# Optimization experiments

Measured on AMD Instinct MI355X. Metric: run time of the kernel, lower is better.

Reference implementation:

```python
import jax, jax.numpy as jnp
import numpy as np

B, S, D, H, HD = 2, 2048, 2048, 16, 128


def precompute_freqs_cis(dim, end, theta=10000.0):
    freqs = 1.0 / theta ** (np.arange(0, dim, 2, dtype=np.float32)[: dim // 2] / dim)
    t = np.arange(end, dtype=np.float32)
    freqs = np.outer(t, freqs)
    freqs = np.concatenate((freqs, freqs), axis=-1)  # [S, HD]
    return jnp.asarray(np.cos(freqs)), jnp.asarray(np.sin(freqs))


def rotate_half(x):
    x1, x2 = x[..., : x.shape[-1] // 2], x[..., x.shape[-1] // 2 :]
    return jnp.concatenate((-x2, x1), axis=-1)


def setup_inputs() -> dict:
    key = jax.random.key(0)
    ks = jax.random.split(key, 5)
    scale = 1.0 / np.sqrt(D)
    return {
        "x": jax.random.normal(ks[0], (B, S, D), jnp.float32),
        "mask": jnp.ones((1, 1, S, S), jnp.bool_),
        "Wq": jax.random.normal(ks[1], (D, H, HD), jnp.float32) * scale,
        "Wk": jax.random.normal(ks[2], (D, H, HD), jnp.float32) * scale,
        "Wv": jax.random.normal(ks[3], (D, H, HD), jnp.float32) * scale,
        "Wo": jax.random.normal(ks[4], (H, HD, D), jnp.float32) * scale,
    }


def reference(x, mask, Wq, Wk, Wv, Wo):
    seq_len = x.shape[1]
    head_dim = Wq.shape[-1]
    # QKV projections: [B,S,D] x [D,H,HD] -> [B,S,H,HD]
    q = jnp.einsum("bsd,dhk->bshk", x, Wq)
    k = jnp.einsum("bsd,dhk->bshk", x, Wk)
    v = jnp.einsum("bsd,dhk->bshk", x, Wv)
    # Rotary position embedding
    cos, sin = precompute_freqs_cis(head_dim, seq_len)
    cos = cos[None, :, None, :]  # [1,S,1,HD]
    sin = sin[None, :, None, :]
    q = q * cos + rotate_half(q) * sin
    k = k * cos + rotate_half(k) * sin
    # Scaled dot-product attention (flax dot_product_attention semantics)
    scores = jnp.einsum("bqhk,bskh->bhqs", q / jnp.sqrt(jnp.float32(head_dim)), k.swapaxes(-1, -2))
    big_neg = jnp.finfo(scores.dtype).min
    scores = jnp.where(mask, scores, big_neg)
    attn = jax.nn.softmax(scores, axis=-1)  # [B,H,S,S]
    ctx = jnp.einsum("bhqs,bshk->bqhk", attn, v)  # [B,S,H,HD]
    # Output projection over (head, head_dim)
    return jnp.einsum("bqhk,hkd->bqd", ctx, Wo)
```

## Files before the change

### kernel.cpp

```cpp
#include <hip/hip_runtime.h>
#include <math.h>

#define Bc   2
#define Sc   2048
#define Dc   2048
#define Hc   16
#define HDc  128
#define BSc  4096
#define HHDc 2048

typedef __bf16 bf16_t;
typedef __bf16 bf16x8 __attribute__((ext_vector_type(8)));
typedef __bf16 bf16x4 __attribute__((ext_vector_type(4)));
typedef float  f32x4  __attribute__((ext_vector_type(4)));

#define AS1(p) ((const __attribute__((address_space(1))) void*)(p))
#define AS3(p) ((__attribute__((address_space(3))) void*)(p))

#define MFMA16(a,b,c) __builtin_amdgcn_mfma_f32_16x16x32_bf16((a),(b),(c),0,0,0)

__global__ void convert_x(const float* __restrict__ x, bf16_t* __restrict__ xb)
{
    const size_t i = ((size_t)blockIdx.x * 256 + threadIdx.x) * 4;
    float4 v = *(const float4*)&x[i];
    bf16x4 o; o[0]=(bf16_t)v.x; o[1]=(bf16_t)v.y; o[2]=(bf16_t)v.z; o[3]=(bf16_t)v.w;
    *(bf16x4*)&xb[i] = o;
}

__global__ __launch_bounds__(256) void transpose_w(const float* __restrict__ in,
                                                   bf16_t* __restrict__ out)
{
    __shared__ float T[64][65];
    const int t = threadIdx.x;
    const int r0 = blockIdx.y * 64, c0 = blockIdx.x * 64;
    #pragma unroll
    for (int i = 0; i < 4; ++i) {
        int row = i * 16 + (t >> 4);
        int c4  = (t & 15) * 4;
        float4 v = *(const float4*)&in[(size_t)(r0 + row) * 2048 + c0 + c4];
        T[row][c4] = v.x; T[row][c4+1] = v.y; T[row][c4+2] = v.z; T[row][c4+3] = v.w;
    }
    __syncthreads();
    #pragma unroll
    for (int i = 0; i < 4; ++i) {
        int orow = i * 16 + (t >> 4);
        int c4   = (t & 15) * 4;
        bf16x4 o;
        #pragma unroll
        for (int j = 0; j < 4; ++j) o[j] = (bf16_t)T[c4 + j][orow];
        *(bf16x4*)&out[(size_t)(c0 + orow) * 2048 + r0 + c4] = o;
    }
}

__global__ __launch_bounds__(256) void prep_vtb(const bf16_t* __restrict__ V,
                                                bf16_t* __restrict__ Vt)
{
    __shared__ float T[64][65];
    const int t = threadIdx.x;
    const int s0 = blockIdx.x * 64;
    const int c0 = blockIdx.y * 64;
    const int bh = blockIdx.z;
    const int b = bh >> 4, h = bh & 15;
    #pragma unroll
    for (int i = 0; i < 4; ++i) {
        int row = i * 16 + (t >> 4);
        int c4  = (t & 15) * 4;
        bf16x4 v = *(const bf16x4*)&V[((size_t)(b * Sc + s0 + row)) * HHDc + h * HDc + c0 + c4];
        #pragma unroll
        for (int j = 0; j < 4; ++j) T[row][c4 + j] = (float)v[j];
    }
    __syncthreads();
    #pragma unroll
    for (int i = 0; i < 4; ++i) {
        int orow = i * 16 + (t >> 4);
        int c4   = (t & 15) * 4;
        bf16x4 o;
        #pragma unroll
        for (int j = 0; j < 4; ++j) o[j] = (bf16_t)T[c4 + j][orow];
        *(bf16x4*)&Vt[((size_t)bh * HDc + c0 + orow) * Sc + s0 + c4] = o;
    }
}

__global__ __launch_bounds__(256) void qkv_gemm(const bf16_t* __restrict__ A,
                                                const bf16_t* __restrict__ Bt,
                                                float* __restrict__ Qf,
                                                float* __restrict__ Kf,
                                                bf16_t* __restrict__ Vb)
{
    __shared__ bf16_t As[128 * 64];
    __shared__ bf16_t Bs[128 * 64];
    const int t = threadIdx.x;
    const int w = t >> 6, l = t & 63;
    const int wm = w >> 1, wn = w & 1;
    const int lane15 = l & 15, quad = l >> 4;
    const int swr = (lane15 & 7) * 8;
    const int m0 = blockIdx.y * 128, n0 = blockIdx.x * 128;

    f32x4 acc[4][4];
    #pragma unroll
    for (int i = 0; i < 4; ++i)
        #pragma unroll
        for (int j = 0; j < 4; ++j)
            #pragma unroll
            for (int c = 0; c < 4; ++c) acc[i][j][c] = 0.f;

    const int srow = w * 8 + (l >> 3);
    const int gk   = ((l & 7) * 8) ^ ((srow & 7) * 8);

    for (int k0 = 0; k0 < 2048; k0 += 64) {
        __syncthreads();
        #pragma unroll
        for (int p = 0; p < 4; ++p) {
            __builtin_amdgcn_global_load_lds(
                AS1(A + (size_t)(m0 + p * 32 + srow) * 2048 + k0 + gk),
                AS3(&As[(p * 32 + w * 8) * 64]), 16, 0, 0);
            __builtin_amdgcn_global_load_lds(
                AS1(Bt + (size_t)(n0 + p * 32 + srow) * 2048 + k0 + gk),
                AS3(&Bs[(p * 32 + w * 8) * 64]), 16, 0, 0);
        }
        __syncthreads();
        #pragma unroll
        for (int ks = 0; ks < 2; ++ks) {
            const int rc = ((ks * 4 + quad) * 8) ^ swr;
            bf16x8 a[4], b[4];
            #pragma unroll
            for (int mt = 0; mt < 4; ++mt)
                a[mt] = *(const bf16x8*)&As[(wm * 64 + mt * 16 + lane15) * 64 + rc];
            #pragma unroll
            for (int nt = 0; nt < 4; ++nt)
                b[nt] = *(const bf16x8*)&Bs[(wn * 64 + nt * 16 + lane15) * 64 + rc];
            #pragma unroll
            for (int mt = 0; mt < 4; ++mt)
                #pragma unroll
                for (int nt = 0; nt < 4; ++nt)
                    acc[mt][nt] = MFMA16(a[mt], b[nt], acc[mt][nt]);
        }
    }

    if (n0 < 4096) {
        float* __restrict__ dst = (n0 < 2048) ? Qf : Kf;
        const int nb = n0 & 2047;
        #pragma unroll
        for (int mt = 0; mt < 4; ++mt)
            #pragma unroll
            for (int nt = 0; nt < 4; ++nt)
                #pragma unroll
                for (int r = 0; r < 4; ++r) {
                    const int gm = m0 + wm * 64 + mt * 16 + quad * 4 + r;
                    const int gn = nb + wn * 64 + nt * 16 + lane15;
                    dst[(size_t)gm * 2048 + gn] = acc[mt][nt][r];
                }
    } else {
        const int nb = n0 - 4096;
        #pragma unroll
        for (int mt = 0; mt < 4; ++mt)
            #pragma unroll
            for (int nt = 0; nt < 4; ++nt)
                #pragma unroll
                for (int r = 0; r < 4; ++r) {
                    const int gm = m0 + wm * 64 + mt * 16 + quad * 4 + r;
                    const int gn = nb + wn * 64 + nt * 16 + lane15;
                    Vb[(size_t)gm * 2048 + gn] = (bf16_t)acc[mt][nt][r];
                }
    }
}

__global__ __launch_bounds__(256) void gemm_bt(const bf16_t* __restrict__ A,
                                               const bf16_t* __restrict__ Bt,
                                               float* __restrict__ C)
{
    __shared__ bf16_t As[128 * 64];
    __shared__ bf16_t Bs[128 * 64];
    const int t = threadIdx.x;
    const int w = t >> 6, l = t & 63;
    const int wm = w >> 1, wn = w & 1;
    const int lane15 = l & 15, quad = l >> 4;
    const int swr = (lane15 & 7) * 8;
    const int m0 = blockIdx.y * 128, n0 = blockIdx.x * 128;

    f32x4 acc[4][4];
    #pragma unroll
    for (int i = 0; i < 4; ++i)
        #pragma unroll
        for (int j = 0; j < 4; ++j)
            #pragma unroll
            for (int c = 0; c < 4; ++c) acc[i][j][c] = 0.f;

    const int srow = w * 8 + (l >> 3);
    const int gk   = ((l & 7) * 8) ^ ((srow & 7) * 8);

    for (int k0 = 0; k0 < 2048; k0 += 64) {
        __syncthreads();
        #pragma unroll
        for (int p = 0; p < 4; ++p) {
            __builtin_amdgcn_global_load_lds(
                AS1(A + (size_t)(m0 + p * 32 + srow) * 2048 + k0 + gk),
                AS3(&As[(p * 32 + w * 8) * 64]), 16, 0, 0);
            __builtin_amdgcn_global_load_lds(
                AS1(Bt + (size_t)(n0 + p * 32 + srow) * 2048 + k0 + gk),
                AS3(&Bs[(p * 32 + w * 8) * 64]), 16, 0, 0);
        }
        __syncthreads();
        #pragma unroll
        for (int ks = 0; ks < 2; ++ks) {
            const int rc = ((ks * 4 + quad) * 8) ^ swr;
            bf16x8 a[4], b[4];
            #pragma unroll
            for (int mt = 0; mt < 4; ++mt)
                a[mt] = *(const bf16x8*)&As[(wm * 64 + mt * 16 + lane15) * 64 + rc];
            #pragma unroll
            for (int nt = 0; nt < 4; ++nt)
                b[nt] = *(const bf16x8*)&Bs[(wn * 64 + nt * 16 + lane15) * 64 + rc];
            #pragma unroll
            for (int mt = 0; mt < 4; ++mt)
                #pragma unroll
                for (int nt = 0; nt < 4; ++nt)
                    acc[mt][nt] = MFMA16(a[mt], b[nt], acc[mt][nt]);
        }
    }

    #pragma unroll
    for (int mt = 0; mt < 4; ++mt)
        #pragma unroll
        for (int nt = 0; nt < 4; ++nt)
            #pragma unroll
            for (int r = 0; r < 4; ++r) {
                const int gm = m0 + wm * 64 + mt * 16 + quad * 4 + r;
                const int gn = n0 + wn * 64 + nt * 16 + lane15;
                C[(size_t)gm * 2048 + gn] = acc[mt][nt][r];
            }
}

__global__ void rope_scale_cast(const float* __restrict__ Qf,
                                const float* __restrict__ Kf,
                                bf16_t* __restrict__ Qh,
                                bf16_t* __restrict__ Kh)
{
    const int idx  = blockIdx.x * 256 + threadIdx.x;
    const int j4   = (idx & 15) * 4;
    const int h    = (idx >> 4) & (Hc - 1);
    const int sabs = idx >> 8;
    const int s    = sabs & (Sc - 1);
    const float QS = 0.08838834764831845f;

    const size_t base = (size_t)sabs * HHDc + (size_t)h * HDc + j4;
    float4 q1 = *(const float4*)&Qf[base];
    float4 q2 = *(const float4*)&Qf[base + 64];
    float4 k1 = *(const float4*)&Kf[base];
    float4 k2 = *(const float4*)&Kf[base + 64];

    bf16x4 qo1, qo2, ko1, ko2;
    #pragma unroll
    for (int c = 0; c < 4; ++c) {
        const float freq = expf(-(float)(j4 + c) * 0.14391156514261520f);
        const float ang  = (float)s * freq;
        float sn, cs;
        sincosf(ang, &sn, &cs);
        const float a = ((const float*)&q1)[c], bq = ((const float*)&q2)[c];
        const float x = ((const float*)&k1)[c], y  = ((const float*)&k2)[c];
        qo1[c] = (bf16_t)((a * cs - bq * sn) * QS);
        qo2[c] = (bf16_t)((bq * cs + a * sn) * QS);
        ko1[c] = (bf16_t)(x * cs - y * sn);
        ko2[c] = (bf16_t)(y * cs + x * sn);
    }
    *(bf16x4*)&Qh[base]      = qo1;
    *(bf16x4*)&Qh[base + 64] = qo2;
    *(bf16x4*)&Kh[base]      = ko1;
    *(bf16x4*)&Kh[base + 64] = ko2;
}

__global__ __launch_bounds__(512, 4) void attn_v6(const bf16_t* __restrict__ Q,
                                                  const bf16_t* __restrict__ K,
                                                  const bf16_t* __restrict__ Vt,
                                                  bf16_t* __restrict__ CTX)
{
    __shared__ bf16_t Ks[64 * 128];
    __shared__ bf16_t Vts[128 * 64];
    __shared__ bf16_t Ps[128 * 72];
    __shared__ float  Arow[128];
    __shared__ float  Lrow[128];

    const int t = threadIdx.x, w = t >> 6, l = t & 63;
    const int lane15 = l & 15, quad = l >> 4;
    const int swr = (lane15 & 7) * 8;
    const int q0 = blockIdx.x * 128;
    const int b = blockIdx.y >> 4, h = blockIdx.y & 15;
    const size_t qbase = ((size_t)(b * Sc + q0)) * HHDc + h * HDc;
    const size_t vtb   = (size_t)blockIdx.y * HDc * Sc;
    const size_t kb0   = ((size_t)(b * Sc)) * HHDc + h * HDc;

    bf16x8 qf[4];
    #pragma unroll
    for (int ks = 0; ks < 4; ++ks)
        qf[ks] = *(const bf16x8*)&Q[qbase
            + (size_t)(w * 16 + lane15) * HHDc + (ks * 4 + quad) * 8];

    float m_[4], l_[4];
    #pragma unroll
    for (int r = 0; r < 4; ++r) { m_[r] = -INFINITY; l_[r] = 0.f; }

    f32x4 O[8];
    #pragma unroll
    for (int i = 0; i < 8; ++i)
        #pragma unroll
        for (int c = 0; c < 4; ++c) O[i][c] = 0.f;

    const int krow0 = w * 4 + (l >> 4);
    const int kgc   = lane15 * 8;
    const int vrow0 = w * 8 + (l >> 3);
    const int vgc   = (l & 7) * 8;

    bf16x8 kst[2], vst[2];
    #pragma unroll
    for (int p = 0; p < 2; ++p) {
        kst[p] = *(const bf16x8*)&K[kb0 + (size_t)(p * 32 + krow0) * HHDc + kgc];
        vst[p] = *(const bf16x8*)&Vt[vtb + (size_t)(p * 64 + vrow0) * Sc + vgc];
    }

    for (int kt = 0; kt < Sc / 64; ++kt) {
        __syncthreads();
        #pragma unroll
        for (int p = 0; p < 2; ++p) {
            const int rk = p * 32 + krow0;
            *(bf16x8*)&Ks[rk * 128 + (kgc ^ ((rk & 7) * 8))] = kst[p];
        }
        #pragma unroll
        for (int p = 0; p < 2; ++p) {
            const int rv = p * 64 + vrow0;
            *(bf16x8*)&Vts[rv * 64 + (vgc ^ ((rv & 7) * 8))] = vst[p];
        }
        if (kt + 1 < Sc / 64) {
            const size_t kbn = kb0 + (size_t)(kt + 1) * 64 * HHDc;
            #pragma unroll
            for (int p = 0; p < 2; ++p) {
                kst[p] = *(const bf16x8*)&K[kbn + (size_t)(p * 32 + krow0) * HHDc + kgc];
                vst[p] = *(const bf16x8*)&Vt[vtb + (size_t)(p * 64 + vrow0) * Sc
                                             + (kt + 1) * 64 + vgc];
            }
        }
        __syncthreads();

        f32x4 sc[4];
        #pragma unroll
        for (int j = 0; j < 4; ++j)
            #pragma unroll
            for (int c = 0; c < 4; ++c) sc[j][c] = 0.f;
        __builtin_amdgcn_s_setprio(1);
        #pragma unroll
        for (int ks = 0; ks < 4; ++ks) {
            const int rc = ((ks * 4 + quad) * 8) ^ swr;
            bf16x8 bk[4];
            #pragma unroll
            for (int nt = 0; nt < 4; ++nt)
                bk[nt] = *(const bf16x8*)&Ks[(nt * 16 + lane15) * 128 + rc];
            #pragma unroll
            for (int nt = 0; nt < 4; ++nt)
                sc[nt] = MFMA16(qf[ks], bk[nt], sc[nt]);
        }
        __builtin_amdgcn_s_setprio(0);

        #pragma unroll
        for (int r = 0; r < 4; ++r) {
            const float v0 = sc[0][r], v1 = sc[1][r];
            const float v2 = sc[2][r], v3 = sc[3][r];
            float tm = fmaxf(fmaxf(v0, v1), fmaxf(v2, v3));
            tm = fmaxf(tm, __shfl_xor(tm, 1));
            tm = fmaxf(tm, __shfl_xor(tm, 2));
            tm = fmaxf(tm, __shfl_xor(tm, 4));
            tm = fmaxf(tm, __shfl_xor(tm, 8));
            const float mo = m_[r];
            const float mn = fmaxf(mo, tm);
            const float al = __expf(mo - mn);
            m_[r] = mn;
            const float p0 = __expf(v0 - mn), p1 = __expf(v1 - mn);
            const float p2 = __expf(v2 - mn), p3 = __expf(v3 - mn);
            float ts = (p0 + p1) + (p2 + p3);
            ts += __shfl_xor(ts, 1);
            ts += __shfl_xor(ts, 2);
            ts += __shfl_xor(ts, 4);
            ts += __shfl_xor(ts, 8);
            l_[r] = l_[r] * al + ts;
            const int qrow = w * 16 + quad * 4 + r;
            Ps[qrow * 72 +  0 + lane15] = (bf16_t)p0;
            Ps[qrow * 72 + 16 + lane15] = (bf16_t)p1;
            Ps[qrow * 72 + 32 + lane15] = (bf16_t)p2;
            Ps[qrow * 72 + 48 + lane15] = (bf16_t)p3;
            if (lane15 == r) Arow[qrow] = al;
        }

        {
            const float al = Arow[w * 16 + lane15];
            #pragma unroll
            for (int ht = 0; ht < 8; ++ht)
                #pragma unroll
                for (int c = 0; c < 4; ++c) O[ht][c] *= al;
        }
        __builtin_amdgcn_s_setprio(1);
        #pragma unroll
        for (int ks = 0; ks < 2; ++ks) {
            const int rcp = (ks * 4 + quad) * 8;
            const int rcv = rcp ^ swr;
            bf16x8 av[8];
            #pragma unroll
            for (int ht = 0; ht < 8; ++ht)
                av[ht] = *(const bf16x8*)&Vts[(ht * 16 + lane15) * 64 + rcv];
            bf16x8 bp = *(const bf16x8*)&Ps[(w * 16 + lane15) * 72 + rcp];
            #pragma unroll
            for (int ht = 0; ht < 8; ++ht)
                O[ht] = MFMA16(av[ht], bp, O[ht]);
        }
        __builtin_amdgcn_s_setprio(0);
    }

    #pragma unroll
    for (int r = 0; r < 4; ++r)
        if (lane15 == r) Lrow[w * 16 + quad * 4 + r] = l_[r];
    __syncthreads();

    {
        const float linv = 1.0f / Lrow[w * 16 + lane15];
        const int s = q0 + w * 16 + lane15;
        #pragma unroll
        for (int ht = 0; ht < 8; ++ht) {
            bf16x4 o;
            #pragma unroll
            for (int c = 0; c < 4; ++c) o[c] = (bf16_t)(O[ht][c] * linv);
            *(bf16x4*)&CTX[((size_t)(b * Sc + s)) * HHDc + h * HDc + ht * 16 + quad * 4] = o;
        }
    }
}

extern "C" void kernel_launch(void* const* d_in, const int* in_sizes, int n_in,
                              void* d_out, int out_size, void* d_ws, size_t ws_size,
                              hipStream_t stream)
{
    const float* x  = (const float*)d_in[0];
    const float* Wq = (const float*)d_in[2];
    const float* Wk = (const float*)d_in[3];
    const float* Wv = (const float*)d_in[4];
    const float* Wo = (const float*)d_in[5];
    float* out = (float*)d_out;

    bf16_t* W0  = (bf16_t*)d_ws;
    bf16_t* xb  = W0;
    bf16_t* WT3 = W0 + 8388608;
    bf16_t* WoT = W0 + 20971520;
    float*  Qf  = (float*)(W0 + 25165824);
    float*  Kf  = (float*)(W0 + 41943040);
    bf16_t* Vb  = W0 + 58720256;
    bf16_t* Kh  = W0;
    bf16_t* Qh  = W0 + 8388608;
    bf16_t* Vt  = W0 + 25165824;
    bf16_t* CTX = W0 + 41943040;

    dim3 tw(32, 32);

    convert_x<<<8192, 256, 0, stream>>>(x, xb);
    transpose_w<<<tw, 256, 0, stream>>>(Wq, WT3);
    transpose_w<<<tw, 256, 0, stream>>>(Wk, WT3 + 4194304);
    transpose_w<<<tw, 256, 0, stream>>>(Wv, WT3 + 8388608);
    transpose_w<<<tw, 256, 0, stream>>>(Wo, WoT);

    qkv_gemm<<<dim3(48, 32), 256, 0, stream>>>(xb, WT3, Qf, Kf, Vb);

    rope_scale_cast<<<4096, 256, 0, stream>>>(Qf, Kf, Qh, Kh);
    prep_vtb<<<dim3(32, 2, 32), 256, 0, stream>>>(Vb, Vt);

    attn_v6<<<dim3(16, 32), 512, 0, stream>>>(Qh, Kh, Vt, CTX);

    gemm_bt<<<dim3(16, 32), 256, 0, stream>>>(CTX, WoT, out);
}
```

Before: 478.4 us.

## Transpose S MFMA so each lane owns a query row; swizzle GEMM block order

The attention kernel swaps the MFMA operand order for QK^T, so S is produced transposed and each lane holds one query row across its registers. Softmax max and sum now reduce mostly within a lane with only two cross-quad shuffles, and the per-row alpha and final l no longer pass through shared memory. That removes the Arow/Lrow arrays and the closing __syncthreads. Separately, both GEMMs remap block IDs with an interleaving swizzle, which changes which tiles run at the same time and is meant to improve L2 reuse.

Result: faster. 441.3 us (-7.8%).

```diff
diff --git a/kernel.cpp b/kernel.cpp
--- a/kernel.cpp
+++ b/kernel.cpp
@@ -94,7 +94,10 @@
     const int wm = w >> 1, wn = w & 1;
     const int lane15 = l & 15, quad = l >> 4;
     const int swr = (lane15 & 7) * 8;
-    const int m0 = blockIdx.y * 128, n0 = blockIdx.x * 128;
+
+    const int id  = blockIdx.y * 48 + blockIdx.x;
+    const int swz = (id & 7) * 192 + (id >> 3);
+    const int m0 = (swz / 48) * 128, n0 = (swz % 48) * 128;
 
     f32x4 acc[4][4];
     #pragma unroll
@@ -176,7 +179,10 @@
     const int wm = w >> 1, wn = w & 1;
     const int lane15 = l & 15, quad = l >> 4;
     const int swr = (lane15 & 7) * 8;
-    const int m0 = blockIdx.y * 128, n0 = blockIdx.x * 128;
+
+    const int id  = blockIdx.y * 16 + blockIdx.x;
+    const int swz = (id & 7) * 64 + (id >> 3);
+    const int m0 = (swz / 16) * 128, n0 = (swz % 16) * 128;
 
     f32x4 acc[4][4];
     #pragma unroll
@@ -269,7 +275,7 @@
     *(bf16x4*)&Kh[base + 64] = ko2;
 }
 
-__global__ __launch_bounds__(512, 4) void attn_v6(const bf16_t* __restrict__ Q,
+__global__ __launch_bounds__(512, 4) void attn_v7(const bf16_t* __restrict__ Q,
                                                   const bf16_t* __restrict__ K,
                                                   const bf16_t* __restrict__ Vt,
                                                   bf16_t* __restrict__ CTX)
@@ -277,8 +283,6 @@
     __shared__ bf16_t Ks[64 * 128];
     __shared__ bf16_t Vts[128 * 64];
     __shared__ bf16_t Ps[128 * 72];
-    __shared__ float  Arow[128];
-    __shared__ float  Lrow[128];
 
     const int t = threadIdx.x, w = t >> 6, l = t & 63;
     const int lane15 = l & 15, quad = l >> 4;
@@ -295,9 +299,7 @@
         qf[ks] = *(const bf16x8*)&Q[qbase
             + (size_t)(w * 16 + lane15) * HHDc + (ks * 4 + quad) * 8];
 
-    float m_[4], l_[4];
-    #pragma unroll
-    for (int r = 0; r < 4; ++r) { m_[r] = -INFINITY; l_[r] = 0.f; }
+    float m_ = -INFINITY, l_ = 0.f;
 
     f32x4 O[8];
     #pragma unroll
@@ -355,46 +357,45 @@
                 bk[nt] = *(const bf16x8*)&Ks[(nt * 16 + lane15) * 128 + rc];
             #pragma unroll
             for (int nt = 0; nt < 4; ++nt)
-                sc[nt] = MFMA16(qf[ks], bk[nt], sc[nt]);
+                sc[nt] = MFMA16(bk[nt], qf[ks], sc[nt]);
         }
         __builtin_amdgcn_s_setprio(0);
 
-        #pragma unroll
-        for (int r = 0; r < 4; ++r) {
-            const float v0 = sc[0][r], v1 = sc[1][r];
-            const float v2 = sc[2][r], v3 = sc[3][r];
-            float tm = fmaxf(fmaxf(v0, v1), fmaxf(v2, v3));
-            tm = fmaxf(tm, __shfl_xor(tm, 1));
-            tm = fmaxf(tm, __shfl_xor(tm, 2));
-            tm = fmaxf(tm, __shfl_xor(tm, 4));
-            tm = fmaxf(tm, __shfl_xor(tm, 8));
-            const float mo = m_[r];
+        {
+            float tm = -INFINITY;
+            #pragma unroll
+            for (int nt = 0; nt < 4; ++nt)
+                #pragma unroll
+                for (int r = 0; r < 4; ++r) tm = fmaxf(tm, sc[nt][r]);
+            tm = fmaxf(tm, __shfl_xor(tm, 16));
+            tm = fmaxf(tm, __shfl_xor(tm, 32));
+            const float mo = m_;
             const float mn = fmaxf(mo, tm);
             const float al = __expf(mo - mn);
-            m_[r] = mn;
-            const float p0 = __expf(v0 - mn), p1 = __expf(v1 - mn);
-            const float p2 = __expf(v2 - mn), p3 = __expf(v3 - mn);
-            float ts = (p0 + p1) + (p2 + p3);
-            ts += __shfl_xor(ts, 1);
-            ts += __shfl_xor(ts, 2);
-            ts += __shfl_xor(ts, 4);
-            ts += __shfl_xor(ts, 8);
-            l_[r] = l_[r] * al + ts;
-            const int qrow = w * 16 + quad * 4 + r;
-            Ps[qrow * 72 +  0 + lane15] = (bf16_t)p0;
-            Ps[qrow * 72 + 16 + lane15] = (bf16_t)p1;
-            Ps[qrow * 72 + 32 + lane15] = (bf16_t)p2;
-            Ps[qrow * 72 + 48 + lane15] = (bf16_t)p3;
-            if (lane15 == r) Arow[qrow] = al;
-        }
-
-        {
-            const float al = Arow[w * 16 + lane15];
+            m_ = mn;
+            float ts = 0.f;
+            const int prow = (w * 16 + lane15) * 72;
+            #pragma unroll
+            for (int nt = 0; nt < 4; ++nt) {
+                bf16x4 pw;
+                #pragma unroll
+                for (int r = 0; r < 4; ++r) {
+                    const float p = __expf(sc[nt][r] - mn);
+                    pw[r] = (bf16_t)p;
+                    ts += p;
+                }
+                *(bf16x4*)&Ps[prow + nt * 16 + quad * 4] = pw;
+            }
+            ts += __shfl_xor(ts, 16);
+            ts += __shfl_xor(ts, 32);
+            l_ = l_ * al + ts;
+
             #pragma unroll
             for (int ht = 0; ht < 8; ++ht)
                 #pragma unroll
                 for (int c = 0; c < 4; ++c) O[ht][c] *= al;
         }
+
         __builtin_amdgcn_s_setprio(1);
         #pragma unroll
         for (int ks = 0; ks < 2; ++ks) {
@@ -412,13 +413,8 @@
         __builtin_amdgcn_s_setprio(0);
     }
 
-    #pragma unroll
-    for (int r = 0; r < 4; ++r)
-        if (lane15 == r) Lrow[w * 16 + quad * 4 + r] = l_[r];
-    __syncthreads();
-
     {
-        const float linv = 1.0f / Lrow[w * 16 + lane15];
+        const float linv = 1.0f / l_;
         const int s = q0 + w * 16 + lane15;
         #pragma unroll
         for (int ht = 0; ht < 8; ++ht) {
@@ -466,7 +462,7 @@
     rope_scale_cast<<<4096, 256, 0, stream>>>(Qf, Kf, Qh, Kh);
     prep_vtb<<<dim3(32, 2, 32), 256, 0, stream>>>(Vb, Vt);
 
-    attn_v6<<<dim3(16, 32), 512, 0, stream>>>(Qh, Kh, Vt, CTX);
+    attn_v7<<<dim3(16, 32), 512, 0, stream>>>(Qh, Kh, Vt, CTX);
 
     gemm_bt<<<dim3(16, 32), 256, 0, stream>>>(CTX, WoT, out);
 }
```
